# Kernel tuning notes

Hardware: AMD Instinct MI355X
Metric: run time of the kernel (lower is better)

The kernel has to match this reference:

```python
import jax, jax.numpy as jnp
import numpy as np

B, L, D = 32, 128, 256  # batch, len_arg, in_dim (== h_dim)
H4 = 4 * D


def setup_inputs() -> dict:
    key = jax.random.key(0)
    k1, k2, k3, k4, k5, k6 = jax.random.split(key, 6)
    arg_1 = jax.random.normal(k1, (B, L, D), dtype=jnp.float32)
    arg_2 = jax.random.normal(k2, (B, L, D), dtype=jnp.float32)
    length_x1 = jax.random.randint(k3, (B,), 1, L + 1, dtype=jnp.int32)
    length_x2 = jax.random.randint(k4, (B,), 1, L + 1, dtype=jnp.int32)
    # xavier-normal-ish params
    fc_w = jax.random.normal(k5, (H4, D), dtype=jnp.float32) * (2.0 / (D + H4)) ** 0.5
    fc_b = jnp.zeros((H4,), dtype=jnp.float32)
    we_w = jax.random.normal(k6, (D,), dtype=jnp.float32) * (2.0 / (D + 1)) ** 0.5
    return {"arg_1": arg_1, "length_x1": length_x1, "arg_2": arg_2,
            "length_x2": length_x2, "fc_w": fc_w, "fc_b": fc_b, "we_w": we_w}


def reference(arg_1, length_x1, arg_2, length_x2, fc_w, fc_b, we_w):
    b, l, d = arg_1.shape
    # pairwise offsets: word_1[i] - word_2[j] -> [B, L, L, D]
    offset = arg_1[:, :, None, :] - arg_2[:, None, :, :]
    # validity mask replaces the per-sample pack+zero-pad (order inside dim 1 is
    # irrelevant: softmax + weighted-sum are permutation invariant, pads are 0)
    idx = jnp.arange(l)
    valid = (idx[None, :, None] < length_x1[:, None, None]) & \
            (idx[None, None, :] < length_x2[:, None, None])          # [B, L, L]
    matrix = jnp.where(valid[..., None], offset, 0.0).reshape(b, l * l, d)
    we = jnp.einsum('bnd,d->bn', matrix, we_w)                        # [B, L*L]
    we_masked = jnp.where(jnp.abs(we) < 1e-7, jnp.float32(-1e7), we)  # masked_fill
    alpha = jax.nn.softmax(we_masked, axis=1)                         # [B, L*L]
    pooled = jnp.einsum('bn,bnd->bd', alpha, matrix)                  # [B, D]
    out = jnp.tanh(pooled @ fc_w.T + fc_b)                            # [B, 4D]
    # dropout(0.5) is identity in eval mode
    return out
```

## Files before the change

### kernel.cpp

```cpp
#include <hip/hip_runtime.h>
#include <math.h>

#define BB 32
#define LL 128
#define DD 256
#define HH 1024
#define A1STRIDE 65

__device__ __forceinline__ float waveReduceSum(float v) {
#pragma unroll
    for (int m = 32; m >= 1; m >>= 1) v += __shfl_xor(v, m, 64);
    return v;
}

__global__ __launch_bounds__(1024) void batch_oct_kernel(
    const float* __restrict__ a1, const int* __restrict__ len1,
    const float* __restrict__ a2, const int* __restrict__ len2,
    const float* __restrict__ fcw, const float* __restrict__ fcb,
    const float* __restrict__ ww, float* __restrict__ out)
{
    const int blk  = blockIdx.x;
    const int b    = blk & 31;
    const int q8   = blk >> 5;
    const int tid  = threadIdx.x;
    const int wave = tid >> 6;
    const int lane = tid & 63;

    __shared__ __align__(16) float4 A1l[LL * A1STRIDE];
    __shared__ __align__(16) float4 wws4[DD / 4];
    __shared__ float s1[LL], s2[LL], E1[LL], E2m[LL];
    __shared__ float rsv[LL], csv[LL];
    __shared__ float part[1024];
    __shared__ float redS[16], redM[16];
    __shared__ __align__(16) float4 ps4[DD / 4];

    const int l1 = len1[b];
    const int l2 = len2[b];

    if (tid < DD / 4) wws4[tid] = ((const float4*)ww)[tid];
    __syncthreads();

    const float* __restrict__ A1 = a1 + (size_t)b * LL * DD;
    const float* __restrict__ A2 = a2 + (size_t)b * LL * DD;

    {
        const int r = tid >> 2;
        const int t = tid & 3;
        float ax = 0.f, ay = 0.f, az = 0.f, aw = 0.f;
        if (r < LL) {
            const float4* __restrict__ row = (const float4*)(A1 + (size_t)r * DD);
#pragma unroll
            for (int qq = 0; qq < 16; ++qq) {
                const int idx = qq * 4 + t;
                const float4 v = row[idx];
                A1l[r * A1STRIDE + idx] = v;
                const float4 w = wws4[idx];
                ax += v.x * w.x; ay += v.y * w.y; az += v.z * w.z; aw += v.w * w.w;
            }
        } else {
            const float4* __restrict__ row = (const float4*)(A2 + (size_t)(r - LL) * DD);
#pragma unroll
            for (int qq = 0; qq < 16; ++qq) {
                const int idx = qq * 4 + t;
                const float4 v = row[idx];
                const float4 w = wws4[idx];
                ax += v.x * w.x; ay += v.y * w.y; az += v.z * w.z; aw += v.w * w.w;
            }
        }
        float s = (ax + ay) + (az + aw);
        s += __shfl_xor(s, 1, 64);
        s += __shfl_xor(s, 2, 64);
        if (t == 0) { if (r < LL) s1[r] = s; else s2[r - LL] = s; }
    }
    __syncthreads();

    {
        float v = 0.f;
        if (tid < LL) {
            const float e = expf(s1[tid]);
            E1[tid] = e;
            if (tid < l1) v = e;
        } else if (tid < 2 * LL) {
            const int j = tid - LL;
            const float e = expf(-s2[j]);
            E2m[j] = e;
            if (j < l2) v = e;
        }
        v = waveReduceSum(v);
        if (lane == 0) redS[wave] = v;
    }
    __syncthreads();
    {
        int cnt = 0;
        const int base = tid * 16;
#pragma unroll
        for (int qq = 0; qq < 16; ++qq) {
            const int n = base + qq;
            const int i = n >> 7, j = n & 127;
            if (i < l1 && j < l2 && fabsf(s1[i] - s2[j]) < 1e-7f) cnt++;
        }
        float fcnt = waveReduceSum((float)cnt);
        if (lane == 0) redM[wave] = fcnt;
    }
    __syncthreads();
    const float S1 = redS[0] + redS[1];
    const float S2 = redS[2] + redS[3];
    float Mtot = 0.f;
#pragma unroll
    for (int w = 0; w < 16; ++w) Mtot += redM[w];
    const float dinv = 1.0f / (S1 * S2 - Mtot);

    {
        const int rr  = tid >> 2;
        const int sub = tid & 3;
        int c2 = 0;
        if (rr < LL) {
            if (rr < l1) {
                const float si = s1[rr];
#pragma unroll 4
                for (int k = 0; k < 32; ++k) {
                    const int j = sub + 4 * k;
                    if (j < l2 && fabsf(si - s2[j]) < 1e-7f) c2++;
                }
            }
        } else {
            const int jj = rr - LL;
            if (jj < l2) {
                const float sj = s2[jj];
#pragma unroll 4
                for (int k = 0; k < 32; ++k) {
                    const int i = sub + 4 * k;
                    if (i < l1 && fabsf(s1[i] - sj) < 1e-7f) c2++;
                }
            }
        }
        c2 += __shfl_xor(c2, 1, 64);
        c2 += __shfl_xor(c2, 2, 64);
        if (sub == 0) {
            if (rr < LL)
                rsv[rr] = (rr < l1) ? (E1[rr] * S2 - (float)c2) * dinv : 0.f;
            else
                csv[rr - LL] = (rr - LL < l2) ? (E2m[rr - LL] * S1 - (float)c2) * dinv : 0.f;
        }
    }
    __syncthreads();

    {
        const int d = tid & 255;
        const int g = tid >> 8;
        const float* __restrict__ A1s = (const float*)A1l;
        float p = 0.f;
#pragma unroll 8
        for (int k = 0; k < 32; ++k) {
            const int i = g * 32 + k;
            p += rsv[i] * A1s[i * (A1STRIDE * 4) + d] - csv[i] * A2[i * DD + d];
        }
        part[tid] = p;
    }
    __syncthreads();
    if (tid < DD) {
        ((float*)ps4)[tid] = part[tid] + part[256 + tid] + part[512 + tid] + part[768 + tid];
    }
    __syncthreads();

    {
        const int hl  = tid >> 4;
        const int t16 = tid & 15;
        const float4 u0 = ps4[t16];
        const float4 u1 = ps4[16 + t16];
        const float4 u2 = ps4[32 + t16];
        const float4 u3 = ps4[48 + t16];
        float* __restrict__ outb = out + (size_t)b * HH;
#pragma unroll
        for (int pass = 0; pass < 2; ++pass) {
            const int h = q8 * 128 + pass * 64 + hl;
            const float4* __restrict__ wrow = (const float4*)(fcw + (size_t)h * DD);
            const float4 v0 = wrow[t16];
            const float4 v1 = wrow[16 + t16];
            const float4 v2 = wrow[32 + t16];
            const float4 v3 = wrow[48 + t16];
            float acc = v0.x * u0.x + v0.y * u0.y + v0.z * u0.z + v0.w * u0.w;
            acc      += v1.x * u1.x + v1.y * u1.y + v1.z * u1.z + v1.w * u1.w;
            acc      += v2.x * u2.x + v2.y * u2.y + v2.z * u2.z + v2.w * u2.w;
            acc      += v3.x * u3.x + v3.y * u3.y + v3.z * u3.z + v3.w * u3.w;
            acc += __shfl_xor(acc, 1, 64);
            acc += __shfl_xor(acc, 2, 64);
            acc += __shfl_xor(acc, 4, 64);
            acc += __shfl_xor(acc, 8, 64);
            if (t16 == 0) outb[h] = tanhf(acc + fcb[h]);
        }
    }
}

extern "C" void kernel_launch(void* const* d_in, const int* in_sizes, int n_in,
                              void* d_out, int out_size, void* d_ws, size_t ws_size,
                              hipStream_t stream) {
    const float* a1   = (const float*)d_in[0];
    const int*   len1 = (const int*)d_in[1];
    const float* a2   = (const float*)d_in[2];
    const int*   len2 = (const int*)d_in[3];
    const float* fcw  = (const float*)d_in[4];
    const float* fcb  = (const float*)d_in[5];
    const float* ww   = (const float*)d_in[6];
    float* out = (float*)d_out;

    batch_oct_kernel<<<256, 1024, 0, stream>>>(a1, len1, a2, len2, fcw, fcb, ww, out);
}
```

Baseline: 16.46 us.

## Derive mask total from per-row counts and vectorize pooled reduction with float4

Drops the separate full L*L pass that counted masked pairs. The total is now rebuilt by summing the per-row match counts that were already being computed. The pooling stage switches from scalar loads over 4 row groups to float4 loads over 16 row groups, with a float4 shared partial buffer. This saves one L*L comparison pass and speeds up the A2 global reads, at the cost of more shared memory and a 16-way final reduction done by 64 threads.

```diff
diff --git a/kernel.cpp b/kernel.cpp
--- a/kernel.cpp
+++ b/kernel.cpp
@@ -27,10 +27,10 @@
     const int lane = tid & 63;
 
     __shared__ __align__(16) float4 A1l[LL * A1STRIDE];
+    __shared__ __align__(16) float4 part4[1024];
     __shared__ __align__(16) float4 wws4[DD / 4];
     __shared__ float s1[LL], s2[LL], E1[LL], E2m[LL];
     __shared__ float rsv[LL], csv[LL];
-    __shared__ float part[1024];
     __shared__ float redS[16], redM[16];
     __shared__ __align__(16) float4 ps4[DD / 4];
 
@@ -90,37 +90,18 @@
         if (lane == 0) redS[wave] = v;
     }
     __syncthreads();
-    {
-        int cnt = 0;
-        const int base = tid * 16;
-#pragma unroll
-        for (int qq = 0; qq < 16; ++qq) {
-            const int n = base + qq;
-            const int i = n >> 7, j = n & 127;
-            if (i < l1 && j < l2 && fabsf(s1[i] - s2[j]) < 1e-7f) cnt++;
-        }
-        float fcnt = waveReduceSum((float)cnt);
-        if (lane == 0) redM[wave] = fcnt;
-    }
-    __syncthreads();
-    const float S1 = redS[0] + redS[1];
-    const float S2 = redS[2] + redS[3];
-    float Mtot = 0.f;
-#pragma unroll
-    for (int w = 0; w < 16; ++w) Mtot += redM[w];
-    const float dinv = 1.0f / (S1 * S2 - Mtot);
 
     {
         const int rr  = tid >> 2;
         const int sub = tid & 3;
-        int c2 = 0;
+        int c = 0;
         if (rr < LL) {
             if (rr < l1) {
                 const float si = s1[rr];
 #pragma unroll 4
                 for (int k = 0; k < 32; ++k) {
                     const int j = sub + 4 * k;
-                    if (j < l2 && fabsf(si - s2[j]) < 1e-7f) c2++;
+                    if (j < l2 && fabsf(si - s2[j]) < 1e-7f) c++;
                 }
             }
         } else {
@@ -130,36 +111,65 @@
 #pragma unroll 4
                 for (int k = 0; k < 32; ++k) {
                     const int i = sub + 4 * k;
-                    if (i < l1 && fabsf(s1[i] - sj) < 1e-7f) c2++;
+                    if (i < l1 && fabsf(s1[i] - sj) < 1e-7f) c++;
                 }
             }
         }
-        c2 += __shfl_xor(c2, 1, 64);
-        c2 += __shfl_xor(c2, 2, 64);
+        c += __shfl_xor(c, 1, 64);
+        c += __shfl_xor(c, 2, 64);
         if (sub == 0) {
-            if (rr < LL)
-                rsv[rr] = (rr < l1) ? (E1[rr] * S2 - (float)c2) * dinv : 0.f;
-            else
-                csv[rr - LL] = (rr - LL < l2) ? (E2m[rr - LL] * S1 - (float)c2) * dinv : 0.f;
-        }
-    }
-    __syncthreads();
-
-    {
-        const int d = tid & 255;
-        const int g = tid >> 8;
-        const float* __restrict__ A1s = (const float*)A1l;
-        float p = 0.f;
-#pragma unroll 8
-        for (int k = 0; k < 32; ++k) {
-            const int i = g * 32 + k;
-            p += rsv[i] * A1s[i * (A1STRIDE * 4) + d] - csv[i] * A2[i * DD + d];
-        }
-        part[tid] = p;
-    }
-    __syncthreads();
-    if (tid < DD) {
-        ((float*)ps4)[tid] = part[tid] + part[256 + tid] + part[512 + tid] + part[768 + tid];
+            if (rr < LL) rsv[rr] = (float)c;
+            else         csv[rr - LL] = (float)c;
+        }
+    }
+    __syncthreads();
+
+    {
+        float mc = (tid < LL && tid < l1) ? rsv[tid] : 0.f;
+        mc = waveReduceSum(mc);
+        if (lane == 0) redM[wave] = mc;
+    }
+    __syncthreads();
+    const float S1 = redS[0] + redS[1];
+    const float S2 = redS[2] + redS[3];
+    const float Mtot = redM[0] + redM[1];
+    const float dinv = 1.0f / (S1 * S2 - Mtot);
+
+    if (tid < LL)
+        rsv[tid] = (tid < l1) ? (E1[tid] * S2 - rsv[tid]) * dinv : 0.f;
+    else if (tid < 2 * LL) {
+        const int j = tid - LL;
+        csv[j] = (j < l2) ? (E2m[j] * S1 - csv[j]) * dinv : 0.f;
+    }
+    __syncthreads();
+
+    {
+        const int d4 = tid & 63;
+        const int g  = tid >> 6;
+        const float4* __restrict__ A2v = (const float4*)A2;
+        float4 acc = make_float4(0.f, 0.f, 0.f, 0.f);
+#pragma unroll
+        for (int k = 0; k < 8; ++k) {
+            const int i = g * 8 + k;
+            const float4 va = A1l[i * A1STRIDE + d4];
+            const float4 vb = A2v[i * 64 + d4];
+            const float r_ = rsv[i], c_ = csv[i];
+            acc.x += r_ * va.x - c_ * vb.x;
+            acc.y += r_ * va.y - c_ * vb.y;
+            acc.z += r_ * va.z - c_ * vb.z;
+            acc.w += r_ * va.w - c_ * vb.w;
+        }
+        part4[tid] = acc;
+    }
+    __syncthreads();
+    if (tid < 64) {
+        float4 p = part4[tid];
+#pragma unroll
+        for (int g2 = 1; g2 < 16; ++g2) {
+            const float4 qv = part4[g2 * 64 + tid];
+            p.x += qv.x; p.y += qv.y; p.z += qv.z; p.w += qv.w;
+        }
+        ps4[tid] = p;
     }
     __syncthreads();
 
```

After: 15.00 us. 1.1x faster.
